# Kernel tuning notes

Measured on AMD Instinct MI355X. Metric: run time of the kernel, lower is better.

The kernel has to match this reference:

```python
import jax, jax.numpy as jnp
import numpy as np

N_NODES = 50000
N_EDGES = 1600000
IN_FEATS = 256
OUT_FEATS = 128
NEG_SLOPE = 0.2


def setup_inputs() -> dict:
    key = jax.random.key(0)
    k1, k2, k3, k4, k5, k6 = jax.random.split(key, 6)
    gain = np.sqrt(2.0)  # calculate_gain('relu')
    w_std = gain * np.sqrt(2.0 / (IN_FEATS + OUT_FEATS))  # xavier normal
    a_std = gain * np.sqrt(2.0 / (1 + OUT_FEATS))
    return {
        "feat": jax.random.normal(k1, (N_NODES, IN_FEATS), dtype=jnp.float32),
        "W": jax.random.normal(k2, (OUT_FEATS, IN_FEATS), dtype=jnp.float32) * w_std,
        "attn_l": jax.random.normal(k3, (1, OUT_FEATS), dtype=jnp.float32) * a_std,
        "attn_r": jax.random.normal(k4, (1, OUT_FEATS), dtype=jnp.float32) * a_std,
        "src": jax.random.randint(k5, (N_EDGES,), 0, N_NODES, dtype=jnp.int32),
        "dst": jax.random.randint(k6, (N_EDGES,), 0, N_NODES, dtype=jnp.int32),
    }


def reference(feat, W, attn_l, attn_r, src, dst):
    # h = fc(feat): [N, D]
    h = jnp.einsum("ni,di->nd", feat, W)
    # per-node attention logits
    el = jnp.sum(h * attn_l, axis=-1)  # [N]
    er = jnp.sum(h * attn_r, axis=-1)  # [N]
    # apply_edge: e_uv = el[u] + er[v], then leaky relu
    e = jax.nn.leaky_relu(el[src] + er[dst], NEG_SLOPE)  # [E]
    # edge softmax over incoming edges of each destination node
    m = jax.ops.segment_max(e, dst, num_segments=N_NODES)  # [N]
    m = jnp.where(jnp.isneginf(m), 0.0, m)  # nodes with no in-edges
    ex = jnp.exp(e - m[dst])  # [E]
    denom = jax.ops.segment_sum(ex, dst, num_segments=N_NODES)  # [N]
    alpha = ex / jnp.maximum(denom[dst], 1e-9)  # [E]
    # gspmv: rst[v] = sum_{(u->v)} alpha_uv * h[u]
    rst = jax.ops.segment_sum(h[src] * alpha[:, None], dst, num_segments=N_NODES)
    return rst
```

## Files before the change

### kernel.cpp

```cpp
#include <hip/hip_runtime.h>
#include <hip/hip_bf16.h>


#define IN_FEATS 256
#define OUT_FEATS 128
#define NBINS 1024
#define BUCK 64
#define CAPB_LOG 12
#define CAPB (1 << CAPB_LOG)
#define SORT_CAP 4096
#define SCAT_BLOCKS 512
#define BIN_STRIDE 16

typedef __bf16 bf16x8 __attribute__((ext_vector_type(8)));
typedef float f32x4 __attribute__((ext_vector_type(4)));

__global__ void prep(const float* __restrict__ W, __bf16* __restrict__ Wb, int nw,
                     int* __restrict__ cur) {
    int i = blockIdx.x * 256 + threadIdx.x;
    if (i < nw) Wb[i] = (__bf16)W[i];
    if (i < NBINS) cur[i * BIN_STRIDE] = i << CAPB_LOG;
}

__global__ __launch_bounds__(256) void gemm_scatter(
    const float* __restrict__ feat, const __bf16* __restrict__ Wb,
    const float* __restrict__ attn_l, const float* __restrict__ attn_r,
    __bf16* __restrict__ hb, float* __restrict__ el, float* __restrict__ er,
    const int* __restrict__ src, const int* __restrict__ dst,
    int* __restrict__ bin_cur, unsigned* __restrict__ arena,
    int n, int E, int G) {
    __shared__ unsigned sorted[SORT_CAP];
    __shared__ int h[NBINS];
    __shared__ int off[NBINS];
    __shared__ int gbase[NBINS];
    __shared__ int sblk[256];

    if (blockIdx.x >= G) {
        const int t = threadIdx.x;
        const int blk = blockIdx.x - G;
        const int chunk = (E + SCAT_BLOCKS - 1) / SCAT_BLOCKS;
        const int beg = blk * chunk;
        const int end = min(beg + chunk, E);

        h[4 * t] = 0; h[4 * t + 1] = 0; h[4 * t + 2] = 0; h[4 * t + 3] = 0;
        __syncthreads();
        for (int i = beg + t; i < end; i += 256)
            atomicAdd(&h[dst[i] >> 6], 1);
        __syncthreads();

        const int a0 = h[4 * t], a1 = h[4 * t + 1], a2 = h[4 * t + 2], a3 = h[4 * t + 3];
        const int tot = a0 + a1 + a2 + a3;
        sblk[t] = tot;
        __syncthreads();
        for (int o = 1; o < 256; o <<= 1) {
            int v = (t >= o) ? sblk[t - o] : 0;
            __syncthreads();
            sblk[t] += v;
            __syncthreads();
        }
        const int base = sblk[t] - tot;
        off[4 * t] = base;
        off[4 * t + 1] = base + a0;
        off[4 * t + 2] = base + a0 + a1;
        off[4 * t + 3] = base + a0 + a1 + a2;
        if (a0 > 0) gbase[4 * t]     = atomicAdd(&bin_cur[(4 * t) * BIN_STRIDE], a0);
        if (a1 > 0) gbase[4 * t + 1] = atomicAdd(&bin_cur[(4 * t + 1) * BIN_STRIDE], a1);
        if (a2 > 0) gbase[4 * t + 2] = atomicAdd(&bin_cur[(4 * t + 2) * BIN_STRIDE], a2);
        if (a3 > 0) gbase[4 * t + 3] = atomicAdd(&bin_cur[(4 * t + 3) * BIN_STRIDE], a3);
        h[4 * t] = 0; h[4 * t + 1] = 0; h[4 * t + 2] = 0; h[4 * t + 3] = 0;
        __syncthreads();

        for (int i = beg + t; i < end; i += 256) {
            int d = dst[i];
            int bin = d >> 6;
            int r = atomicAdd(&h[bin], 1);
            sorted[off[bin] + r] = ((unsigned)d << 16) | (unsigned)src[i];
        }
        __syncthreads();

        const int tot2 = end - beg;
        for (int j = t; j < tot2; j += 256) {
            unsigned w = sorted[j];
            int bin = w >> 22;
            int pos = gbase[bin] + (j - off[bin]);
            pos = min(pos, ((bin + 1) << CAPB_LOG) - 1);
            arena[pos] = w;
        }
        return;
    }

    const int wid = threadIdx.x >> 6;
    const int lane = threadIdx.x & 63;
    const int s = lane & 15;
    const int q = lane >> 4;
    const int m0 = blockIdx.x * 64 + wid * 16;
    if (m0 >= n) return;

    const int mrow = min(m0 + s, n - 1);
    const float* arow = feat + (size_t)mrow * IN_FEATS + q * 8;

    f32x4 acc[8];
#pragma unroll
    for (int nt = 0; nt < 8; nt++) acc[nt] = (f32x4){0.f, 0.f, 0.f, 0.f};

#pragma unroll
    for (int ks = 0; ks < 8; ks++) {
        const int k0 = ks * 32;
        float4 f0 = *(const float4*)(arow + k0);
        float4 f1 = *(const float4*)(arow + k0 + 4);
        bf16x8 a;
        a[0] = (__bf16)f0.x; a[1] = (__bf16)f0.y; a[2] = (__bf16)f0.z; a[3] = (__bf16)f0.w;
        a[4] = (__bf16)f1.x; a[5] = (__bf16)f1.y; a[6] = (__bf16)f1.z; a[7] = (__bf16)f1.w;
#pragma unroll
        for (int nt = 0; nt < 8; nt++) {
            bf16x8 b = *(const bf16x8*)(Wb + (size_t)(nt * 16 + s) * IN_FEATS + k0 + q * 8);
            acc[nt] = __builtin_amdgcn_mfma_f32_16x16x32_bf16(a, b, acc[nt], 0, 0, 0);
        }
    }

    float al[8], ar[8];
#pragma unroll
    for (int nt = 0; nt < 8; nt++) {
        al[nt] = attn_l[nt * 16 + s];
        ar[nt] = attn_r[nt * 16 + s];
    }

#pragma unroll
    for (int r = 0; r < 4; r++) {
        const int row = m0 + q * 4 + r;
        const bool ok = row < n;
        float pl = 0.f, pr = 0.f;
#pragma unroll
        for (int nt = 0; nt < 8; nt++) {
            float v = acc[nt][r];
            if (ok) hb[(size_t)row * OUT_FEATS + nt * 16 + s] = (__bf16)v;
            pl += v * al[nt];
            pr += v * ar[nt];
        }
#pragma unroll
        for (int m = 1; m < 16; m <<= 1) {
            pl += __shfl_xor(pl, m);
            pr += __shfl_xor(pr, m);
        }
        if (ok && s == 0) {
            el[row] = pl;
            er[row] = pr;
        }
    }
}

__global__ __launch_bounds__(512) void csr_gat(
    const unsigned* __restrict__ arena, const int* __restrict__ bin_cur,
    const float* __restrict__ el, const float* __restrict__ er,
    const __bf16* __restrict__ hb, float* __restrict__ out, int N) {
    __shared__ unsigned stage[CAPB];
    __shared__ int cnt[BUCK];
    __shared__ int off[BUCK];
    __shared__ float erl[BUCK];
    const int b = blockIdx.x;
    const int t = threadIdx.x;
    const int abeg = b << CAPB_LOG;
    const int cin = min(bin_cur[b * BIN_STRIDE] - abeg, CAPB);
    const int d0 = b * BUCK;

    if (t < BUCK) {
        cnt[t] = 0;
        erl[t] = (d0 + t < N) ? er[d0 + t] : 0.f;
    }
    __syncthreads();

    for (int i = t; i < cin; i += 512)
        atomicAdd(&cnt[(arena[abeg + i] >> 16) & (BUCK - 1)], 1);
    __syncthreads();
    if (t < BUCK) off[t] = cnt[t];
    __syncthreads();
    for (int o = 1; o < BUCK; o <<= 1) {
        int v = (t < BUCK && t >= o) ? off[t - o] : 0;
        __syncthreads();
        if (t < BUCK) off[t] += v;
        __syncthreads();
    }
    if (t < BUCK) {
        off[t] -= cnt[t];
        cnt[t] = 0;
    }
    __syncthreads();

    for (int i = t; i < cin; i += 512) {
        unsigned e = arena[abeg + i];
        int d6 = (e >> 16) & (BUCK - 1);
        int u = (int)(e & 0xFFFFu);
        float x = el[u] + erl[d6];
        x = (x > 0.f) ? x : 0.2f * x;
        float w = __expf(x);
        int r = atomicAdd(&cnt[d6], 1);
        stage[off[d6] + r] = (__float_as_uint(w) & 0xFFFF0000u) | (unsigned)u;
    }
    __syncthreads();

    const int wid = t >> 6;
    const int lane = t & 63;
    const unsigned* hbu = (const unsigned*)hb;
#pragma unroll 1
    for (int j = 0; j < BUCK / 8; j++) {
        const int d6 = wid * (BUCK / 8) + j;
        const int v = d0 + d6;
        if (v >= N) break;
        const int rbeg = __builtin_amdgcn_readfirstlane(off[d6]);
        const int deg  = __builtin_amdgcn_readfirstlane(cnt[d6]);
        float acc0 = 0.f, acc1 = 0.f, wsum = 0.f;
        for (int c0 = rbeg; c0 < rbeg + deg; c0 += 64) {
            const int nn = min(64, rbeg + deg - c0);
            unsigned my = (lane < nn) ? stage[c0 + lane] : 0u;
            int k = 0;
            for (; k + 8 <= nn; k += 8) {
#pragma unroll
                for (int tt = 0; tt < 8; tt++) {
                    const unsigned es = (unsigned)__builtin_amdgcn_readlane((int)my, k + tt);
                    const unsigned us = es & 0xFFFFu;
                    const float ws = __uint_as_float(es & 0xFFFF0000u);
                    const unsigned pair = hbu[(size_t)us * (OUT_FEATS / 2) + lane];
                    wsum += ws;
                    acc0 += ws * __uint_as_float(pair << 16);
                    acc1 += ws * __uint_as_float(pair & 0xffff0000u);
                }
            }
            for (; k < nn; k++) {
                const unsigned es = (unsigned)__builtin_amdgcn_readlane((int)my, k);
                const unsigned us = es & 0xFFFFu;
                const float ws = __uint_as_float(es & 0xFFFF0000u);
                const unsigned pair = hbu[(size_t)us * (OUT_FEATS / 2) + lane];
                wsum += ws;
                acc0 += ws * __uint_as_float(pair << 16);
                acc1 += ws * __uint_as_float(pair & 0xffff0000u);
            }
        }
        const float dnm = fmaxf(wsum, 1e-9f);
        float2 o = make_float2(acc0 / dnm, acc1 / dnm);
        *(float2*)(out + (size_t)v * OUT_FEATS + lane * 2) = o;
    }
}

extern "C" void kernel_launch(void* const* d_in, const int* in_sizes, int n_in,
                              void* d_out, int out_size, void* d_ws, size_t ws_size,
                              hipStream_t stream) {
    const float* feat   = (const float*)d_in[0];
    const float* W      = (const float*)d_in[1];
    const float* attn_l = (const float*)d_in[2];
    const float* attn_r = (const float*)d_in[3];
    const int*   src    = (const int*)d_in[4];
    const int*   dst    = (const int*)d_in[5];
    const int N = in_sizes[0] / IN_FEATS;
    const int E = in_sizes[4];
    float* out = (float*)d_out;

    char* p = (char*)d_ws;
    auto alloc = [&](size_t bytes) -> char* {
        char* r = p;
        p += (bytes + 255) & ~(size_t)255;
        return r;
    };
    const int nbuckets = (N + BUCK - 1) / BUCK;

    __bf16* hb      = (__bf16*)alloc((size_t)N * OUT_FEATS * sizeof(__bf16));
    __bf16* Wb      = (__bf16*)alloc((size_t)OUT_FEATS * IN_FEATS * sizeof(__bf16));
    float*  el      = (float*)alloc((size_t)N * sizeof(float));
    float*  er      = (float*)alloc((size_t)N * sizeof(float));
    int*    bin_cur = (int*)alloc((size_t)NBINS * BIN_STRIDE * sizeof(int));
    unsigned* arena = (unsigned*)alloc((size_t)NBINS * CAPB * sizeof(unsigned));

    const int nw = OUT_FEATS * IN_FEATS;
    prep<<<dim3((nw + 255) / 256), dim3(256), 0, stream>>>(W, Wb, nw, bin_cur);

    const int G = (N + 63) / 64;
    gemm_scatter<<<dim3(G + SCAT_BLOCKS), dim3(256), 0, stream>>>(
        feat, Wb, attn_l, attn_r, hb, el, er, src, dst, bin_cur, arena, N, E, G);

    csr_gat<<<dim3(nbuckets), dim3(512), 0, stream>>>(arena, bin_cur, el, er,
                                                      hb, out, N);
}
```

Baseline: 218.6 us.

## Split each CSR bin across two blocks and prefetch GEMM A-rows up front

```diff
diff --git a/kernel.cpp b/kernel.cpp
--- a/kernel.cpp
+++ b/kernel.cpp
@@ -11,6 +11,7 @@
 #define SORT_CAP 4096
 #define SCAT_BLOCKS 512
 #define BIN_STRIDE 16
+#define STAGE_CAP 2560
 
 typedef __bf16 bf16x8 __attribute__((ext_vector_type(8)));
 typedef float f32x4 __attribute__((ext_vector_type(4)));
@@ -99,6 +100,21 @@
     const int mrow = min(m0 + s, n - 1);
     const float* arow = feat + (size_t)mrow * IN_FEATS + q * 8;
 
+    float4 f[16];
+#pragma unroll
+    for (int i = 0; i < 8; i++) {
+        f[2 * i]     = *(const float4*)(arow + i * 32);
+        f[2 * i + 1] = *(const float4*)(arow + i * 32 + 4);
+    }
+    bf16x8 av[8];
+#pragma unroll
+    for (int i = 0; i < 8; i++) {
+        av[i][0] = (__bf16)f[2 * i].x;     av[i][1] = (__bf16)f[2 * i].y;
+        av[i][2] = (__bf16)f[2 * i].z;     av[i][3] = (__bf16)f[2 * i].w;
+        av[i][4] = (__bf16)f[2 * i + 1].x; av[i][5] = (__bf16)f[2 * i + 1].y;
+        av[i][6] = (__bf16)f[2 * i + 1].z; av[i][7] = (__bf16)f[2 * i + 1].w;
+    }
+
     f32x4 acc[8];
 #pragma unroll
     for (int nt = 0; nt < 8; nt++) acc[nt] = (f32x4){0.f, 0.f, 0.f, 0.f};
@@ -106,15 +122,10 @@
 #pragma unroll
     for (int ks = 0; ks < 8; ks++) {
         const int k0 = ks * 32;
-        float4 f0 = *(const float4*)(arow + k0);
-        float4 f1 = *(const float4*)(arow + k0 + 4);
-        bf16x8 a;
-        a[0] = (__bf16)f0.x; a[1] = (__bf16)f0.y; a[2] = (__bf16)f0.z; a[3] = (__bf16)f0.w;
-        a[4] = (__bf16)f1.x; a[5] = (__bf16)f1.y; a[6] = (__bf16)f1.z; a[7] = (__bf16)f1.w;
 #pragma unroll
         for (int nt = 0; nt < 8; nt++) {
             bf16x8 b = *(const bf16x8*)(Wb + (size_t)(nt * 16 + s) * IN_FEATS + k0 + q * 8);
-            acc[nt] = __builtin_amdgcn_mfma_f32_16x16x32_bf16(a, b, acc[nt], 0, 0, 0);
+            acc[nt] = __builtin_amdgcn_mfma_f32_16x16x32_bf16(av[ks], b, acc[nt], 0, 0, 0);
         }
     }
 
@@ -153,34 +164,38 @@
     const unsigned* __restrict__ arena, const int* __restrict__ bin_cur,
     const float* __restrict__ el, const float* __restrict__ er,
     const __bf16* __restrict__ hb, float* __restrict__ out, int N) {
-    __shared__ unsigned stage[CAPB];
-    __shared__ int cnt[BUCK];
-    __shared__ int off[BUCK];
-    __shared__ float erl[BUCK];
+    __shared__ unsigned stage[STAGE_CAP];
+    __shared__ int cnt[32];
+    __shared__ int off[32];
+    __shared__ float erl[32];
     const int b = blockIdx.x;
+    const int bin = b >> 1;
+    const int half = b & 1;
     const int t = threadIdx.x;
-    const int abeg = b << CAPB_LOG;
-    const int cin = min(bin_cur[b * BIN_STRIDE] - abeg, CAPB);
-    const int d0 = b * BUCK;
-
-    if (t < BUCK) {
+    const int abeg = bin << CAPB_LOG;
+    const int cin = min(bin_cur[bin * BIN_STRIDE] - abeg, CAPB);
+    const int d0 = bin * BUCK + half * 32;
+
+    if (t < 32) {
         cnt[t] = 0;
         erl[t] = (d0 + t < N) ? er[d0 + t] : 0.f;
     }
     __syncthreads();
 
-    for (int i = t; i < cin; i += 512)
-        atomicAdd(&cnt[(arena[abeg + i] >> 16) & (BUCK - 1)], 1);
-    __syncthreads();
-    if (t < BUCK) off[t] = cnt[t];
-    __syncthreads();
-    for (int o = 1; o < BUCK; o <<= 1) {
-        int v = (t < BUCK && t >= o) ? off[t - o] : 0;
-        __syncthreads();
-        if (t < BUCK) off[t] += v;
-        __syncthreads();
-    }
-    if (t < BUCK) {
+    for (int i = t; i < cin; i += 512) {
+        int d6 = (arena[abeg + i] >> 16) & (BUCK - 1);
+        if ((d6 >> 5) == half) atomicAdd(&cnt[d6 & 31], 1);
+    }
+    __syncthreads();
+    if (t < 32) off[t] = cnt[t];
+    __syncthreads();
+    for (int o = 1; o < 32; o <<= 1) {
+        int v = (t < 32 && t >= o) ? off[t - o] : 0;
+        __syncthreads();
+        if (t < 32) off[t] += v;
+        __syncthreads();
+    }
+    if (t < 32) {
         off[t] -= cnt[t];
         cnt[t] = 0;
     }
@@ -189,12 +204,14 @@
     for (int i = t; i < cin; i += 512) {
         unsigned e = arena[abeg + i];
         int d6 = (e >> 16) & (BUCK - 1);
+        if ((d6 >> 5) != half) continue;
         int u = (int)(e & 0xFFFFu);
-        float x = el[u] + erl[d6];
+        float x = el[u] + erl[d6 & 31];
         x = (x > 0.f) ? x : 0.2f * x;
         float w = __expf(x);
-        int r = atomicAdd(&cnt[d6], 1);
-        stage[off[d6] + r] = (__float_as_uint(w) & 0xFFFF0000u) | (unsigned)u;
+        int r = atomicAdd(&cnt[d6 & 31], 1);
+        int pos = min(off[d6 & 31] + r, STAGE_CAP - 1);
+        stage[pos] = (__float_as_uint(w) & 0xFFFF0000u) | (unsigned)u;
     }
     __syncthreads();
 
@@ -202,16 +219,16 @@
     const int lane = t & 63;
     const unsigned* hbu = (const unsigned*)hb;
 #pragma unroll 1
-    for (int j = 0; j < BUCK / 8; j++) {
-        const int d6 = wid * (BUCK / 8) + j;
-        const int v = d0 + d6;
+    for (int j = 0; j < 4; j++) {
+        const int dd = wid * 4 + j;
+        const int v = d0 + dd;
         if (v >= N) break;
-        const int rbeg = __builtin_amdgcn_readfirstlane(off[d6]);
-        const int deg  = __builtin_amdgcn_readfirstlane(cnt[d6]);
+        const int rbeg = __builtin_amdgcn_readfirstlane(off[dd]);
+        const int deg  = __builtin_amdgcn_readfirstlane(cnt[dd]);
         float acc0 = 0.f, acc1 = 0.f, wsum = 0.f;
         for (int c0 = rbeg; c0 < rbeg + deg; c0 += 64) {
             const int nn = min(64, rbeg + deg - c0);
-            unsigned my = (lane < nn) ? stage[c0 + lane] : 0u;
+            unsigned my = (lane < nn) ? stage[min(c0 + lane, STAGE_CAP - 1)] : 0u;
             int k = 0;
             for (; k + 8 <= nn; k += 8) {
 #pragma unroll
@@ -276,6 +293,6 @@
     gemm_scatter<<<dim3(G + SCAT_BLOCKS), dim3(256), 0, stream>>>(
         feat, Wb, attn_l, attn_r, hb, el, er, src, dst, bin_cur, arena, N, E, G);
 
-    csr_gat<<<dim3(nbuckets), dim3(512), 0, stream>>>(arena, bin_cur, el, er,
-                                                      hb, out, N);
-}
+    csr_gat<<<dim3(2 * nbuckets), dim3(512), 0, stream>>>(arena, bin_cur, el, er,
+                                                          hb, out, N);
+}
```

Result: no change. 218.0 us (-0.3%).

## Split bf16 node features into column chunks for cache-local gathers

Applied to the files above, without the earlier changes.

```diff
diff --git a/kernel.cpp b/kernel.cpp
--- a/kernel.cpp
+++ b/kernel.cpp
@@ -99,6 +99,21 @@
     const int mrow = min(m0 + s, n - 1);
     const float* arow = feat + (size_t)mrow * IN_FEATS + q * 8;
 
+    float4 f[16];
+#pragma unroll
+    for (int i = 0; i < 8; i++) {
+        f[2 * i]     = *(const float4*)(arow + i * 32);
+        f[2 * i + 1] = *(const float4*)(arow + i * 32 + 4);
+    }
+    bf16x8 av[8];
+#pragma unroll
+    for (int i = 0; i < 8; i++) {
+        av[i][0] = (__bf16)f[2 * i].x;     av[i][1] = (__bf16)f[2 * i].y;
+        av[i][2] = (__bf16)f[2 * i].z;     av[i][3] = (__bf16)f[2 * i].w;
+        av[i][4] = (__bf16)f[2 * i + 1].x; av[i][5] = (__bf16)f[2 * i + 1].y;
+        av[i][6] = (__bf16)f[2 * i + 1].z; av[i][7] = (__bf16)f[2 * i + 1].w;
+    }
+
     f32x4 acc[8];
 #pragma unroll
     for (int nt = 0; nt < 8; nt++) acc[nt] = (f32x4){0.f, 0.f, 0.f, 0.f};
@@ -106,15 +121,10 @@
 #pragma unroll
     for (int ks = 0; ks < 8; ks++) {
         const int k0 = ks * 32;
-        float4 f0 = *(const float4*)(arow + k0);
-        float4 f1 = *(const float4*)(arow + k0 + 4);
-        bf16x8 a;
-        a[0] = (__bf16)f0.x; a[1] = (__bf16)f0.y; a[2] = (__bf16)f0.z; a[3] = (__bf16)f0.w;
-        a[4] = (__bf16)f1.x; a[5] = (__bf16)f1.y; a[6] = (__bf16)f1.z; a[7] = (__bf16)f1.w;
 #pragma unroll
         for (int nt = 0; nt < 8; nt++) {
             bf16x8 b = *(const bf16x8*)(Wb + (size_t)(nt * 16 + s) * IN_FEATS + k0 + q * 8);
-            acc[nt] = __builtin_amdgcn_mfma_f32_16x16x32_bf16(a, b, acc[nt], 0, 0, 0);
+            acc[nt] = __builtin_amdgcn_mfma_f32_16x16x32_bf16(av[ks], b, acc[nt], 0, 0, 0);
         }
     }
 
@@ -125,6 +135,7 @@
         ar[nt] = attn_r[nt * 16 + s];
     }
 
+    const size_t chunkElems = (size_t)n * 32;
 #pragma unroll
     for (int r = 0; r < 4; r++) {
         const int row = m0 + q * 4 + r;
@@ -133,7 +144,9 @@
 #pragma unroll
         for (int nt = 0; nt < 8; nt++) {
             float v = acc[nt][r];
-            if (ok) hb[(size_t)row * OUT_FEATS + nt * 16 + s] = (__bf16)v;
+            if (ok)
+                hb[(size_t)(nt >> 1) * chunkElems + (size_t)row * 32 +
+                   ((nt & 1) * 16 + s)] = (__bf16)v;
             pl += v * al[nt];
             pr += v * ar[nt];
         }
@@ -200,44 +213,47 @@
 
     const int wid = t >> 6;
     const int lane = t & 63;
+    const int g = lane >> 4;
+    const int l = lane & 15;
     const unsigned* hbu = (const unsigned*)hb;
+    const size_t chunkWords = (size_t)N * 16;
+
+    for (int c = 0; c < 4; c++) {
+        const unsigned* hc = hbu + (size_t)c * chunkWords;
 #pragma unroll 1
-    for (int j = 0; j < BUCK / 8; j++) {
-        const int d6 = wid * (BUCK / 8) + j;
-        const int v = d0 + d6;
-        if (v >= N) break;
-        const int rbeg = __builtin_amdgcn_readfirstlane(off[d6]);
-        const int deg  = __builtin_amdgcn_readfirstlane(cnt[d6]);
-        float acc0 = 0.f, acc1 = 0.f, wsum = 0.f;
-        for (int c0 = rbeg; c0 < rbeg + deg; c0 += 64) {
-            const int nn = min(64, rbeg + deg - c0);
-            unsigned my = (lane < nn) ? stage[c0 + lane] : 0u;
-            int k = 0;
-            for (; k + 8 <= nn; k += 8) {
-#pragma unroll
-                for (int tt = 0; tt < 8; tt++) {
-                    const unsigned es = (unsigned)__builtin_amdgcn_readlane((int)my, k + tt);
-                    const unsigned us = es & 0xFFFFu;
-                    const float ws = __uint_as_float(es & 0xFFFF0000u);
-                    const unsigned pair = hbu[(size_t)us * (OUT_FEATS / 2) + lane];
-                    wsum += ws;
-                    acc0 += ws * __uint_as_float(pair << 16);
-                    acc1 += ws * __uint_as_float(pair & 0xffff0000u);
+        for (int j = 0; j < BUCK / 8; j++) {
+            const int d6 = wid * (BUCK / 8) + j;
+            const int v = d0 + d6;
+            if (v >= N) break;
+            const int rbeg = __builtin_amdgcn_readfirstlane(off[d6]);
+            const int deg  = __builtin_amdgcn_readfirstlane(cnt[d6]);
+            float a0 = 0.f, a1 = 0.f, ws = 0.f;
+            for (int c0 = rbeg; c0 < rbeg + deg; c0 += 64) {
+                const int nn = min(64, rbeg + deg - c0);
+                unsigned my = (lane < nn) ? stage[c0 + lane] : 0u;
+                for (int k = 0; k < nn; k += 8) {
+                    unsigned e0 = (unsigned)__shfl((int)my, k + g);
+                    unsigned e1 = (unsigned)__shfl((int)my, k + 4 + g);
+                    float w0 = __uint_as_float(e0 & 0xFFFF0000u);
+                    float w1 = __uint_as_float(e1 & 0xFFFF0000u);
+                    unsigned p0 = hc[(size_t)(e0 & 0xFFFFu) * 16 + l];
+                    unsigned p1 = hc[(size_t)(e1 & 0xFFFFu) * 16 + l];
+                    ws += w0 + w1;
+                    a0 += w0 * __uint_as_float(p0 << 16)
+                        + w1 * __uint_as_float(p1 << 16);
+                    a1 += w0 * __uint_as_float(p0 & 0xffff0000u)
+                        + w1 * __uint_as_float(p1 & 0xffff0000u);
                 }
             }
-            for (; k < nn; k++) {
-                const unsigned es = (unsigned)__builtin_amdgcn_readlane((int)my, k);
-                const unsigned us = es & 0xFFFFu;
-                const float ws = __uint_as_float(es & 0xFFFF0000u);
-                const unsigned pair = hbu[(size_t)us * (OUT_FEATS / 2) + lane];
-                wsum += ws;
-                acc0 += ws * __uint_as_float(pair << 16);
-                acc1 += ws * __uint_as_float(pair & 0xffff0000u);
+            a0 += __shfl_xor(a0, 16); a0 += __shfl_xor(a0, 32);
+            a1 += __shfl_xor(a1, 16); a1 += __shfl_xor(a1, 32);
+            ws += __shfl_xor(ws, 16); ws += __shfl_xor(ws, 32);
+            if (lane < 16) {
+                const float dnm = fmaxf(ws, 1e-9f);
+                *(float2*)(out + (size_t)v * OUT_FEATS + c * 32 + l * 2) =
+                    make_float2(a0 / dnm, a1 / dnm);
             }
         }
-        const float dnm = fmaxf(wsum, 1e-9f);
-        float2 o = make_float2(acc0 / dnm, acc1 / dnm);
-        *(float2*)(out + (size_t)v * OUT_FEATS + lane * 2) = o;
     }
 }
 
```

Result: slower. 246.3 us (+12.7%).
